# Kernel tuning notes

Measured on AMD Instinct MI355X. Metric: run time of the kernel, lower is better.

## Reference

```python
import jax, jax.numpy as jnp
import numpy as np

N_NODES = 15000
N_EDGES = 60000
D_NODE_IN = 74
D_EDGE_IN = 12
D = 64            # node_out_feats
D_EHID = 128      # edge_hidden_feats
N_STEPS = 6
BN_EPS = 1e-5


def setup_inputs() -> dict:
    key = jax.random.key(0)
    ks = jax.random.split(key, 16)
    def lin(k, fan_in, shape):
        return jax.random.normal(k, shape, jnp.float32) / np.sqrt(fan_in)
    inp = {
        "node_feats": jax.random.normal(ks[0], (N_NODES, D_NODE_IN), jnp.float32),
        "edge_feats": jax.random.normal(ks[1], (N_EDGES, D_EDGE_IN), jnp.float32),
        "src": jax.random.randint(ks[2], (N_EDGES,), 0, N_NODES, jnp.int32),
        "dst": jax.random.randint(ks[3], (N_EDGES,), 0, N_NODES, jnp.int32),
        # project_node_feats: Linear(node_in, D)
        "W_proj": lin(ks[4], D_NODE_IN, (D_NODE_IN, D)),
        "b_proj": jnp.zeros((D,), jnp.float32),
        # edge network: Linear(edge_in, ehid) -> ReLU -> Linear(ehid, D*D)
        "W_e1": lin(ks[5], D_EDGE_IN, (D_EDGE_IN, D_EHID)),
        "b_e1": jnp.zeros((D_EHID,), jnp.float32),
        "W_e2": lin(ks[6], D_EHID, (D_EHID, D * D)),
        "b_e2": jnp.zeros((D * D,), jnp.float32),
        # NNConv bias + BatchNorm affine params
        "conv_bias": jnp.zeros((D,), jnp.float32),
        "bn_gamma": jnp.ones((D,), jnp.float32),
        "bn_beta": jnp.zeros((D,), jnp.float32),
        # GRU (single layer): torch layout W_ih [3D, D], W_hh [3D, D]
        "W_ih": lin(ks[7], D, (3 * D, D)),
        "W_hh": lin(ks[8], D, (3 * D, D)),
        "b_ih": jnp.zeros((3 * D,), jnp.float32),
        "b_hh": jnp.zeros((3 * D,), jnp.float32),
    }
    return inp


def reference(node_feats, edge_feats, W_proj, b_proj, W_e1, b_e1, W_e2, b_e2,
              conv_bias, bn_gamma, bn_beta, W_ih, W_hh, b_ih, b_hh, src, dst):
    n_nodes = node_feats.shape[0]

    # project_node_feats: Linear + ReLU
    h = jax.nn.relu(node_feats @ W_proj + b_proj)          # [N, D]
    hidden = h                                              # GRU hidden state

    # edge MLP is a pure function of static edge_feats -> compute once
    ew = jax.nn.relu(edge_feats @ W_e1 + b_e1) @ W_e2 + b_e2
    ew = ew.reshape(-1, D, D)                               # [E, D, D]

    # mean-aggregation normalizer (DGL mean: 0 for isolated nodes)
    deg = jax.ops.segment_sum(jnp.ones_like(dst, jnp.float32), dst,
                              num_segments=n_nodes)
    inv_deg = jnp.where(deg > 0, 1.0 / jnp.maximum(deg, 1.0), 0.0)[:, None]

    for _ in range(N_STEPS):
        # per-edge matvec message: (h_src^T W_e); sum over d_in commutes
        # with the mean reduction, so reduce vectors instead of matrices.
        msg = jnp.einsum('ei,eio->eo', h[src], ew)          # [E, D]
        rst = jax.ops.segment_sum(msg, dst, num_segments=n_nodes) * inv_deg
        rst = rst + conv_bias
        # BatchNorm1d (training mode: batch statistics, biased variance)
        mu = rst.mean(axis=0)
        var = rst.var(axis=0)
        rst = (rst - mu) * jax.lax.rsqrt(var + BN_EPS) * bn_gamma + bn_beta
        m = jax.nn.relu(rst)
        # GRU cell (torch gate order: r, z, n)
        gi = m @ W_ih.T + b_ih
        gh = hidden @ W_hh.T + b_hh
        i_r, i_z, i_n = jnp.split(gi, 3, axis=-1)
        h_r, h_z, h_n = jnp.split(gh, 3, axis=-1)
        r = jax.nn.sigmoid(i_r + h_r)
        z = jax.nn.sigmoid(i_z + h_z)
        n = jnp.tanh(i_n + r * h_n)
        hidden = (1.0 - z) * n + z * hidden
        h = hidden
    return h
```

## Files before the change

### kernel.cpp

```cpp
#include <hip/hip_runtime.h>
#include <hip/hip_bf16.h>
#include <math.h>

#define NN 15000
#define NE 60000
#define DIN 74
#define DEIN 12
#define DD 64
#define EH 128
#define NG 8192
#define NSTEPS 6
#define NRB 235
#define NGB 235
#define KAB 384
#define NTMAX 18752
#define NFB 586

typedef unsigned short ushort_t;
typedef __attribute__((ext_vector_type(8))) short short8v;
typedef __attribute__((ext_vector_type(4))) float float4v;

__device__ __forceinline__ float bsf(unsigned short u){
  union { unsigned int i; float f; } v; v.i = ((unsigned int)u) << 16; return v.f;
}
__device__ __forceinline__ unsigned short fsb(float f){
  union { float f; unsigned int i; } v; v.f = f;
  unsigned int x = v.i;
  return (unsigned short)((x + 0x7FFFu + ((x >> 16) & 1u)) >> 16);
}
__device__ __forceinline__ unsigned int pkbf(float a, float b){
  __hip_bfloat162 r = __float22bfloat162_rn(make_float2(a, b));
  union { __hip_bfloat162 h; unsigned int u; } v; v.h = r; return v.u;
}

__global__ void k_sniff(const ushort_t* __restrict__ nf16,
                        const int* __restrict__ dsti, int* __restrict__ flags){
  __shared__ int cnt[2];
  int t = threadIdx.x;
  if (t < 2) cnt[t] = 0;
  __syncthreads();
  int bad = 0;
  for (int i = t; i < 1024; i += 256){
    unsigned short u = nf16[2*i];
    int e = (u >> 7) & 0xFF;
    if (e < 96 || e > 159) bad++;
  }
  if (bad) atomicAdd(&cnt[0], bad);
  if (t < 256 && dsti[2*t+1] == 0) atomicAdd(&cnt[1], 1);
  __syncthreads();
  if (t == 0){
    flags[0] = (cnt[0] > 300) ? 1 : 0;
    flags[1] = (cnt[1] > 250) ? 1 : 0;
  }
}

struct CanonArgs {
  const void* in[15];
  float* out[15];
  int n[15];
};
__global__ void k_canon_all(CanonArgs a, const int* __restrict__ flags){
  int j = blockIdx.y;
  int n = a.n[j];
  int fp32 = flags[0];
  const void* in = a.in[j];
  float* out = a.out[j];
  for (int i = blockIdx.x*256 + threadIdx.x; i < n; i += gridDim.x*256){
    if (fp32) out[i] = ((const float*)in)[i];
    else      out[i] = bsf(((const ushort_t*)in)[i]);
  }
}
__global__ void k_canoni2(const void* __restrict__ in0, const void* __restrict__ in1,
                          int* __restrict__ out0, int* __restrict__ out1,
                          const int* __restrict__ flags){
  int i = blockIdx.x*256 + threadIdx.x;
  if (i >= NE) return;
  const void* in = blockIdx.y ? in1 : in0;
  int* out = blockIdx.y ? out1 : out0;
  long long v = flags[1] ? ((const long long*)in)[i]
                         : (long long)((const int*)in)[i];
  int vi = (int)v;
  if (vi < 0) vi = 0;
  if (vi >= NN) vi = NN-1;
  out[i] = vi;
}

__global__ void k_proj(const float* __restrict__ nf, const float* __restrict__ Wp,
                       const float* __restrict__ bp, float* __restrict__ hid,
                       ushort_t* __restrict__ ab){
  __shared__ float nfl[4][DIN];
  int t = threadIdx.x, blk = blockIdx.x;
  for (int idx = t; idx < 4*DIN; idx += 256){
    int vl = idx / DIN, i = idx - vl*DIN;
    nfl[vl][i] = nf[(size_t)(blk*4+vl)*DIN + i];
  }
  __syncthreads();
  int vl = t >> 6, o = t & 63;
  int v = blk*4 + vl;
  float acc = bp[o];
  for (int i = 0; i < DIN; ++i) acc += nfl[vl][i] * Wp[i*DD + o];
  float r = fmaxf(acc, 0.f);
  hid[(size_t)v*DD + o] = r;
  ushort_t hh = fsb(r);
  float hl = r - bsf(hh);
  ab[(size_t)v*KAB + 64 + o]  = hh;
  ab[(size_t)v*KAB + 192 + o] = fsb(hl);
  ab[(size_t)v*KAB + 320 + o] = hh;
}

__global__ void k_emlp(const float* __restrict__ ef, const float* __restrict__ W1,
                       const float* __restrict__ b1, ushort_t* __restrict__ thi,
                       ushort_t* __restrict__ tlo){
  __shared__ float efl[2][DEIN];
  int t = threadIdx.x, blk = blockIdx.x;
  if (t < 2*DEIN){
    int el = t / DEIN, i = t - el*DEIN;
    efl[el][i] = ef[(size_t)(blk*2+el)*DEIN + i];
  }
  __syncthreads();
  int el = t >> 7, c = t & 127;
  float acc = b1[c];
  for (int i = 0; i < DEIN; ++i) acc += efl[el][i] * W1[i*EH + c];
  float tv = fmaxf(acc, 0.f);
  ushort_t hiv = fsb(tv);
  size_t off = (size_t)(blk*2+el)*EH + c;
  thi[off] = hiv;
  tlo[off] = fsb(tv - bsf(hiv));
}
__global__ void k_zpad(ushort_t* __restrict__ thi, ushort_t* __restrict__ tlo){
  int t = threadIdx.x;
  thi[(size_t)NE*EH + t] = 0;
  tlo[(size_t)NE*EH + t] = 0;
}

__global__ void k_w2q(const float* __restrict__ W2, const float* __restrict__ b2,
                      ushort_t* __restrict__ w2q, ushort_t* __restrict__ w2b){
  int idx = blockIdx.x*256 + threadIdx.x;
  if (idx < NG*DD){
    int n = idx >> 6, i = idx & 63;
    int kq = n >> 11, rem = n & 2047;
    int o = rem >> 5, kl = rem & 31;
    int kg = kq*32 + kl;
    w2q[idx] = fsb(W2[(size_t)kg*4096 + i*64 + o]);
  } else if (idx < NG*DD + DD*DD){
    int r = idx - NG*DD;
    int o = r >> 6, i = r & 63;
    w2b[r] = fsb(b2[i*64 + o]);
  }
}

__global__ void k_wgru(const float* __restrict__ Wih, const float* __restrict__ Whh,
                       ushort_t* __restrict__ wg){
  int pos = blockIdx.x*256 + threadIdx.x;
  if (pos >= 256*KAB) return;
  int c = pos / KAB, k = pos - c*KAB;
  int kb = k >> 6, i = k & 63;
  int g = c >> 6, o = c & 63;
  float w = 0.f;
  if ((kb & 1) == 0){
    if (g == 0)      w = Wih[(size_t)(o)*64 + i];
    else if (g == 1) w = Wih[(size_t)(64+o)*64 + i];
    else if (g == 2) w = Wih[(size_t)(128+o)*64 + i];
  } else {
    if (g == 0)      w = Whh[(size_t)(o)*64 + i];
    else if (g == 1) w = Whh[(size_t)(64+o)*64 + i];
    else if (g == 3) w = Whh[(size_t)(128+o)*64 + i];
  }
  ushort_t hi = fsb(w);
  wg[pos] = (kb >= 4) ? fsb(w - bsf(hi)) : hi;
}

__global__ void k_zero(int* __restrict__ p, int n){
  int i = blockIdx.x*256 + threadIdx.x;
  if (i < n) p[i] = 0;
}
__global__ void k_deg2(const int* __restrict__ a0, const int* __restrict__ a1,
                       int* __restrict__ d0, int* __restrict__ d1){
  int e = blockIdx.x*256 + threadIdx.x;
  if (e < NE){
    if (blockIdx.y == 0) atomicAdd(&d0[a0[e]], 1);
    else                 atomicAdd(&d1[a1[e]], 1);
  }
}
__global__ void k_scan2(const int* __restrict__ degA, int* __restrict__ rowpA,
                        float* __restrict__ invdA,
                        const int* __restrict__ degB, int* __restrict__ rowpB,
                        float* __restrict__ invdB){
  const int* deg = blockIdx.x ? degB : degA;
  int* rowp      = blockIdx.x ? rowpB : rowpA;
  float* invd    = blockIdx.x ? invdB : invdA;
  __shared__ int ssum[256];
  int t = threadIdx.x;
  const int STRIP = (NN + 255) / 256;
  int lo = t*STRIP, hi = (lo + STRIP < NN) ? lo + STRIP : NN;
  int s = 0;
  for (int i = lo; i < hi; ++i) s += deg[i];
  ssum[t] = s;
  __syncthreads();
  if (t == 0){
    int acc = 0;
    for (int i = 0; i < 256; ++i){ int v = ssum[i]; ssum[i] = acc; acc += v; }
  }
  __syncthreads();
  int acc = ssum[t];
  for (int i = lo; i < hi; ++i){
    rowp[i] = acc;
    int d = deg[i];
    invd[i] = (d > 0) ? 1.0f/(float)d : 0.0f;
    acc += d;
  }
  if (t == 255) rowp[NN] = acc;
}
__global__ void k_scatter2(const int* __restrict__ dstc, const int* __restrict__ rowpD,
                           int* __restrict__ curD, int* __restrict__ eidxD,
                           int* __restrict__ epos,
                           const int* __restrict__ srcc, const int* __restrict__ rowpS,
                           int* __restrict__ curS, int* __restrict__ eidxS){
  int e = blockIdx.x*256 + threadIdx.x;
  if (e >= NE) return;
  if (blockIdx.y == 0){
    int d = dstc[e];
    int pos = atomicAdd(&curD[d], 1);
    int slot = rowpD[d] + pos;
    eidxD[slot] = e;
    epos[e] = slot;
  } else {
    int d = srcc[e];
    int pos = atomicAdd(&curS[d], 1);
    eidxS[rowpS[d] + pos] = e;
  }
}

__global__ void k_tiles(const int* __restrict__ rowp, int* __restrict__ tnode,
                        int* __restrict__ tbase, int* __restrict__ tcnt,
                        int* __restrict__ ntb){
  __shared__ int ss[256];
  int t = threadIdx.x;
  const int STRIP = (NN + 255) / 256;
  int lo = t*STRIP, hi = lo + STRIP; if (hi > NN) hi = NN;
  int c = 0;
  for (int i = lo; i < hi; ++i){
    int deg = rowp[i+1] - rowp[i];
    c += (deg + 15) >> 4;
  }
  ss[t] = c;
  __syncthreads();
  if (t == 0){
    int a = 0;
    for (int i = 0; i < 256; ++i){ int v = ss[i]; ss[i] = a; a += v; }
    ntb[0] = a;
  }
  __syncthreads();
  int pos = ss[t];
  for (int i = lo; i < hi; ++i){
    int b = rowp[i], deg = rowp[i+1] - b;
    for (int r = 0; r < deg; r += 16){
      tnode[pos] = i; tbase[pos] = b + r;
      int c2 = deg - r; tcnt[pos] = (c2 > 16) ? 16 : c2;
      ++pos;
    }
  }
}

__global__ __launch_bounds__(512,4) void k_fused7(
    const ushort_t* __restrict__ ab, const ushort_t* __restrict__ w2q,
    const ushort_t* __restrict__ w2b, const ushort_t* __restrict__ thi,
    const ushort_t* __restrict__ tlo,
    const int* __restrict__ tnode, const int* __restrict__ tbase,
    const int* __restrict__ tcnt, const int* __restrict__ ntb,
    const int* __restrict__ eidx, const int* __restrict__ epos,
    float* __restrict__ msg){
  __shared__ __align__(16) ushort_t Gl[32768];
  __shared__ float bhl[32*66];
  __shared__ int nodl[32], cntl[32], basel[32];
  __shared__ int eidl[32][16];
  __shared__ int posl[32][16];

  int tid = threadIdx.x;
  int nt = ntb[0];
  int T0 = blockIdx.x * 32;
  if (T0 >= nt) return;
  int wv = tid >> 6, lane = tid & 63;
  int lr = lane & 15, quad = lane >> 4;

  if (tid < 32){
    int gt = T0 + tid;
    int node = 0, base = 0, cnt = 0;
    if (gt < nt){ node = tnode[gt]; base = tbase[gt]; cnt = tcnt[gt]; }
    nodl[tid] = node; basel[tid] = base; cntl[tid] = cnt;
  }
  __syncthreads();
  {
    int j = tid >> 4, sl = tid & 15;
    int eid = NE, ps = 0;
    if (sl < cntl[j]){
      eid = eidx[basel[j] + sl];
      ps = epos[eid];
    }
    eidl[j][sl] = eid;
    posl[j][sl] = ps;
  }
  short8v hf0k0, hf0k1, hf1k0, hf1k1;
  {
    int n0 = nodl[lr], n1 = nodl[16 + lr];
    hf0k0 = *(const short8v*)(ab + (size_t)n0*KAB + 64 + quad*8);
    hf0k1 = *(const short8v*)(ab + (size_t)n0*KAB + 96 + quad*8);
    hf1k0 = *(const short8v*)(ab + (size_t)n1*KAB + 64 + quad*8);
    hf1k1 = *(const short8v*)(ab + (size_t)n1*KAB + 96 + quad*8);
  }
  {
    int ot = wv & 3, mh = wv >> 2;
    float4v ba = (float4v){0.f,0.f,0.f,0.f};
    short8v a0 = *(const short8v*)(w2b + (size_t)(ot*16 + lr)*DD + quad*8);
    short8v a1 = *(const short8v*)(w2b + (size_t)(ot*16 + lr)*DD + 32 + quad*8);
    ba = __builtin_amdgcn_mfma_f32_16x16x32_bf16(a0, mh ? hf1k0 : hf0k0, ba, 0,0,0);
    ba = __builtin_amdgcn_mfma_f32_16x16x32_bf16(a1, mh ? hf1k1 : hf0k1, ba, 0,0,0);
    #pragma unroll
    for (int reg = 0; reg < 4; ++reg)
      bhl[(mh*16 + lr)*66 + ot*16 + quad*4 + reg] = ba[reg];
  }

  int j0 = wv*4;
  for (int oh = 0; oh < 2; ++oh){
    float4v acc[4][2];
    #pragma unroll
    for (int j = 0; j < 4; ++j)
      #pragma unroll
      for (int ot = 0; ot < 2; ++ot)
        acc[j][ot] = (float4v){0.f,0.f,0.f,0.f};
    for (int kq = 0; kq < 4; ++kq){
      __syncthreads();
      #pragma unroll 4
      for (int it = 0; it < 8; ++it){
        int tile = wv*8 + it;
        int nrow = kq*2048 + oh*1024 + tile*16 + lr;
        const ushort_t* arow = w2q + (size_t)nrow*DD;
        short8v a0 = *(const short8v*)(arow + quad*8);
        short8v a1 = *(const short8v*)(arow + 32 + quad*8);
        int ol = tile >> 1;
        int klb = ((tile & 1) << 4) + quad*4;
        int q8 = klb >> 3, jj = klb & 7;
        #pragma unroll
        for (int mh = 0; mh < 2; ++mh){
          float4v g = (float4v){0.f,0.f,0.f,0.f};
          g = __builtin_amdgcn_mfma_f32_16x16x32_bf16(a0, mh ? hf1k0 : hf0k0, g, 0,0,0);
          g = __builtin_amdgcn_mfma_f32_16x16x32_bf16(a1, mh ? hf1k1 : hf0k1, g, 0,0,0);
          int m = mh*16 + lr;
          unsigned int p0 = pkbf(g[0], g[1]);
          unsigned int p1 = pkbf(g[2], g[3]);
          int byt = ((((m*4 + q8)*32 + ol) << 4) + jj*2) ^ ((m & 7) << 4);
          uint2 pv; pv.x = p0; pv.y = p1;
          *(uint2*)((char*)Gl + byt) = pv;
        }
      }
      short8v th0, th1, th2, th3, tw0, tw1, tw2, tw3;
      {
        size_t kqo = (size_t)kq*32 + quad*8;
        int e0 = eidl[j0+0][lr], e1 = eidl[j0+1][lr];
        int e2 = eidl[j0+2][lr], e3 = eidl[j0+3][lr];
        th0 = *(const short8v*)(thi + (size_t)e0*EH + kqo);
        tw0 = *(const short8v*)(tlo + (size_t)e0*EH + kqo);
        th1 = *(const short8v*)(thi + (size_t)e1*EH + kqo);
        tw1 = *(const short8v*)(tlo + (size_t)e1*EH + kqo);
        th2 = *(const short8v*)(thi + (size_t)e2*EH + kqo);
        tw2 = *(const short8v*)(tlo + (size_t)e2*EH + kqo);
        th3 = *(const short8v*)(thi + (size_t)e3*EH + kqo);
        tw3 = *(const short8v*)(tlo + (size_t)e3*EH + kqo);
      }
      __syncthreads();
      #pragma unroll
      for (int j = 0; j < 4; ++j){
        int m = j0 + j;
        int swz = (m & 7) << 4;
        short8v thj = (j==0)?th0:(j==1)?th1:(j==2)?th2:th3;
        short8v twj = (j==0)?tw0:(j==1)?tw1:(j==2)?tw2:tw3;
        #pragma unroll
        for (int ot = 0; ot < 2; ++ot){
          int byt = (((m*4 + quad)*32 + ot*16 + lr) << 4) ^ swz;
          short8v gf = *(const short8v*)((const char*)Gl + byt);
          acc[j][ot] = __builtin_amdgcn_mfma_f32_16x16x32_bf16(thj, gf, acc[j][ot], 0,0,0);
          acc[j][ot] = __builtin_amdgcn_mfma_f32_16x16x32_bf16(twj, gf, acc[j][ot], 0,0,0);
        }
      }
    }
    #pragma unroll
    for (int j = 0; j < 4; ++j){
      int m = j0 + j;
      #pragma unroll
      for (int ot = 0; ot < 2; ++ot){
        int o = oh*32 + ot*16 + lr;
        float bb = bhl[m*66 + o];
        #pragma unroll
        for (int reg = 0; reg < 4; ++reg){
          int sl = quad*4 + reg;
          int eid = eidl[m][sl];
          if (eid < NE) msg[(size_t)posl[m][sl]*DD + o] = acc[j][ot][reg] + bb;
        }
      }
    }
  }
}

__global__ __launch_bounds__(512) void k_red(const float* __restrict__ msg,
                      const int* __restrict__ rowp_d,
                      const float* __restrict__ invd, const float* __restrict__ cbias,
                      float* __restrict__ rst, float* __restrict__ part){
  __shared__ float ls[512], ls2[512];
  int t = threadIdx.x, blk = blockIdx.x;
  int o = t & 63, gg = t >> 6;
  float cb = cbias[o];
  float s = 0.f, s2 = 0.f;
  int nbase = blk*64 + gg*8;
  int rp[9];
  #pragma unroll
  for (int k = 0; k < 9; ++k){
    int idx = nbase + k; if (idx > NN) idx = NN;
    rp[k] = rowp_d[idx];
  }
  #pragma unroll 1
  for (int j = 0; j < 8; ++j){
    int n = nbase + j;
    if (n >= NN) break;
    int b = rp[j], e = rp[j+1];
    float a0 = 0.f, a1 = 0.f, a2 = 0.f, a3 = 0.f;
    int i = b;
    for (; i + 3 < e; i += 4){
      a0 += msg[(size_t)i*DD + o];
      a1 += msg[(size_t)(i+1)*DD + o];
      a2 += msg[(size_t)(i+2)*DD + o];
      a3 += msg[(size_t)(i+3)*DD + o];
    }
    for (; i < e; ++i) a0 += msg[(size_t)i*DD + o];
    float x = ((a0 + a1) + (a2 + a3)) * invd[n] + cb;
    rst[(size_t)n*DD + o] = x;
    s += x; s2 += x*x;
  }
  ls[t] = s; ls2[t] = s2;
  __syncthreads();
  if (t < 64){
    float a = 0.f;
    #pragma unroll
    for (int g = 0; g < 8; ++g) a += ls[g*64 + t];
    part[blk*128 + t] = a;
  } else if (t < 128){
    int o2 = t - 64;
    float a = 0.f;
    #pragma unroll
    for (int g = 0; g < 8; ++g) a += ls2[g*64 + o2];
    part[blk*128 + 64 + o2] = a;
  }
}

__global__ __launch_bounds__(512) void k_gru_one(
    const float* __restrict__ rst, const float* __restrict__ part,
    const float* __restrict__ gamma, const float* __restrict__ beta,
    ushort_t* __restrict__ ab, const ushort_t* __restrict__ wg,
    const float* __restrict__ bih, const float* __restrict__ bhh,
    float* __restrict__ hid, float* __restrict__ out, int write_out){
  __shared__ __align__(16) ushort_t As[64][136];
  __shared__ __align__(16) ushort_t Bs[256][136];
  __shared__ float gl[64*257];
  __shared__ float scl[64], sft[64];
  __shared__ float shp[4][128];
  int t = threadIdx.x;
  int r0 = blockIdx.x * 64;
  {
    int tg = t >> 7, tc = t & 127;
    float s0 = 0.f, s1 = 0.f;
    int b = tg;
    for (; b + 4 < NRB; b += 8){ s0 += part[b*128 + tc]; s1 += part[(b+4)*128 + tc]; }
    for (; b < NRB; b += 4) s0 += part[b*128 + tc];
    shp[tg][tc] = s0 + s1;
  }
  __syncthreads();
  if (t < 64){
    float su = shp[0][t] + shp[1][t] + shp[2][t] + shp[3][t];
    float sq = shp[0][64+t] + shp[1][64+t] + shp[2][64+t] + shp[3][64+t];
    float mu = su / (float)NN;
    float var = sq / (float)NN - mu*mu;
    if (var < 0.f) var = 0.f;
    float rsq = rsqrtf(var + 1e-5f);
    float sc = rsq * gamma[t];
    scl[t] = sc;
    sft[t] = beta[t] - mu*sc;
  }
  int wv = t >> 6, lane = t & 63;
  int lr = lane & 15, quad = lane >> 4;
  int n0 = wv * 32;
  float4v acc[4][2];
  #pragma unroll
  for (int mt = 0; mt < 4; ++mt)
    #pragma unroll
    for (int nt = 0; nt < 2; ++nt) acc[mt][nt] = (float4v){0.f,0.f,0.f,0.f};
  for (int kt = 0; kt < 3; ++kt){
    __syncthreads();
    #pragma unroll
    for (int it = 0; it < 2; ++it){
      int cid = t + it*512;
      int r = cid >> 4, ko = (cid & 15) * 8;
      int gm = r0 + r; if (gm >= NN) gm = NN-1;
      if (ko < 64){
        float4 x0 = *(const float4*)(rst + (size_t)gm*DD + ko);
        float4 x1 = *(const float4*)(rst + (size_t)gm*DD + ko + 4);
        float xv[8] = {x0.x,x0.y,x0.z,x0.w,x1.x,x1.y,x1.z,x1.w};
        ushort_t u[8];
        #pragma unroll
        for (int jj = 0; jj < 8; ++jj){
          float m = fmaxf(xv[jj]*scl[ko+jj] + sft[ko+jj], 0.f);
          ushort_t mh = fsb(m);
          u[jj] = (kt == 1) ? fsb(m - bsf(mh)) : mh;
        }
        *(uint4*)&As[r][ko] = *(const uint4*)u;
      } else {
        *(uint4*)&As[r][ko] = *(const uint4*)(ab + (size_t)gm*KAB + kt*128 + ko);
      }
    }
    #pragma unroll
    for (int it = 0; it < 8; ++it){
      int cid = t + it*512;
      int rB = cid >> 4, ko = (cid & 15) * 8;
      *(uint4*)&Bs[rB][ko] = *(const uint4*)(wg + (size_t)rB*KAB + kt*128 + ko);
    }
    __syncthreads();
    #pragma unroll
    for (int ks = 0; ks < 4; ++ks){
      short8v a[4];
      #pragma unroll
      for (int mt = 0; mt < 4; ++mt)
        a[mt] = *(const short8v*)&As[mt*16 + lr][ks*32 + quad*8];
      #pragma unroll
      for (int nt = 0; nt < 2; ++nt){
        short8v b = *(const short8v*)&Bs[n0 + nt*16 + lr][ks*32 + quad*8];
        #pragma unroll
        for (int mt = 0; mt < 4; ++mt)
          acc[mt][nt] = __builtin_amdgcn_mfma_f32_16x16x32_bf16(a[mt], b, acc[mt][nt], 0,0,0);
      }
    }
  }
  #pragma unroll
  for (int mt = 0; mt < 4; ++mt)
    #pragma unroll
    for (int nt = 0; nt < 2; ++nt){
      int col = n0 + nt*16 + lr;
      #pragma unroll
      for (int reg = 0; reg < 4; ++reg)
        gl[(mt*16 + quad*4 + reg)*257 + col] = acc[mt][nt][reg];
    }
  __syncthreads();
  for (int idx = t; idx < 64*64; idx += 512){
    int row = idx >> 6, o = idx & 63;
    int v = r0 + row;
    if (v >= NN) break;
    const float* g = &gl[row*257];
    float aR  = g[o]       + bih[o]      + bhh[o];
    float aZ  = g[64 + o]  + bih[64+o]   + bhh[64+o];
    float aNi = g[128 + o] + bih[128+o];
    float aNh = g[192 + o] + bhh[128+o];
    float hprev = hid[(size_t)v*DD + o];
    float r = 1.f/(1.f+__expf(-aR));
    float z = 1.f/(1.f+__expf(-aZ));
    float n = tanhf(aNi + r*aNh);
    float hnew = (1.f - z)*n + z*hprev;
    hid[(size_t)v*DD + o] = hnew;
    ushort_t hh = fsb(hnew);
    float hl = hnew - bsf(hh);
    ab[(size_t)v*KAB + 64 + o]  = hh;
    ab[(size_t)v*KAB + 192 + o] = fsb(hl);
    ab[(size_t)v*KAB + 320 + o] = hh;
    if (write_out) out[(size_t)v*DD + o] = hnew;
  }
}

extern "C" void kernel_launch(void* const* d_in, const int* in_sizes, int n_in,
                              void* d_out, int out_size, void* d_ws, size_t ws_size,
                              hipStream_t stream){
  (void)out_size; (void)ws_size;
  float* out = (float*)d_out;

  int p_nf=-1,p_ef=-1,p_src=-1,p_dst=-1,p_Wp=-1,p_bp=-1,p_W1=-1,p_b1=-1,
      p_W2=-1,p_b2=-1,p_cb=-1,p_gam=-1,p_bet=-1,p_Wih=-1,p_Whh=-1,p_bih=-1,p_bhh=-1;
  int c60000=0,c64=0,c12288=0,c192=0;
  for (int i = 0; i < n_in; ++i){
    switch (in_sizes[i]){
      case 1110000: p_nf = i; break;
      case 720000:  p_ef = i; break;
      case 60000:   if (c60000++ == 0) p_src = i; else p_dst = i; break;
      case 4736:    p_Wp = i; break;
      case 64:      { if (c64==0) p_bp=i; else if (c64==1) p_cb=i;
                      else if (c64==2) p_gam=i; else p_bet=i; c64++; } break;
      case 1536:    p_W1 = i; break;
      case 128:     p_b1 = i; break;
      case 524288:  p_W2 = i; break;
      case 4096:    p_b2 = i; break;
      case 12288:   if (c12288++ == 0) p_Wih = i; else p_Whh = i; break;
      case 192:    if (c192++ == 0) p_bih = i; else p_bhh = i; break;
      default: break;
    }
  }

  char* p = (char*)d_ws;
  auto alloc = [&](size_t bytes)->char*{
    char* r = p; p += (bytes + 255) & ~(size_t)255; return r;
  };
  int* flags = (int*)alloc(256);
  const int FPOS[15] = {p_nf,p_ef,p_Wp,p_bp,p_W1,p_b1,p_W2,p_b2,p_cb,p_gam,p_bet,
                        p_Wih,p_Whh,p_bih,p_bhh};
  CanonArgs ca;
  int maxn = 0;
  for (int j = 0; j < 15; ++j){
    int n = in_sizes[FPOS[j]];
    ca.in[j]  = d_in[FPOS[j]];
    ca.out[j] = (float*)alloc((size_t)n * 4);
    ca.n[j]   = n;
    if (n > maxn) maxn = n;
  }
  const float* nf  = ca.out[0];  const float* ef  = ca.out[1];
  const float* Wp  = ca.out[2];  const float* bp  = ca.out[3];
  const float* W1  = ca.out[4];  const float* b1  = ca.out[5];
  const float* W2  = ca.out[6];  const float* b2  = ca.out[7];
  const float* cb  = ca.out[8];  const float* gam = ca.out[9];
  const float* bet = ca.out[10]; const float* Wih = ca.out[11];
  const float* Whh = ca.out[12]; const float* bih = ca.out[13];
  const float* bhh = ca.out[14];
  int* srcc = (int*)alloc((size_t)NE*4);
  int* dstc = (int*)alloc((size_t)NE*4);

  ushort_t* thi   = (ushort_t*)alloc((size_t)(NE+1)*EH*2);
  ushort_t* tlo   = (ushort_t*)alloc((size_t)(NE+1)*EH*2);
  ushort_t* w2q   = (ushort_t*)alloc((size_t)NG*DD*2);
  ushort_t* w2b   = (ushort_t*)alloc((size_t)DD*DD*2);
  float* hid      = (float*)alloc((size_t)NN*DD*4);
  ushort_t* ab    = (ushort_t*)alloc((size_t)NN*KAB*2);
  ushort_t* wg    = (ushort_t*)alloc((size_t)256*KAB*2);
  float* rst      = (float*)alloc((size_t)NN*DD*4);
  float* msg      = (float*)alloc((size_t)NE*DD*4);
  float* part     = (float*)alloc((size_t)NRB*128*4);
  int* degall     = (int*)alloc((size_t)4*NN*4);
  int* deg  = degall;
  int* curd = degall + NN;
  int* deg2 = degall + 2*NN; int* cursor2 = degall + 3*NN;
  float* invd = (float*)alloc((size_t)NN*4);
  int* rowp_d = (int*)alloc((size_t)(NN+1)*4);
  int* eidx_d = (int*)alloc((size_t)NE*4);
  int* epos   = (int*)alloc((size_t)NE*4);
  int* rowp2  = (int*)alloc((size_t)(NN+1)*4);
  float* invd2= (float*)alloc((size_t)NN*4);
  int* eidx2  = (int*)alloc((size_t)NE*4);
  int* tnode  = (int*)alloc((size_t)NTMAX*4);
  int* tbase  = (int*)alloc((size_t)NTMAX*4);
  int* tcnt   = (int*)alloc((size_t)NTMAX*4);
  int* ntb    = (int*)alloc(256);

  k_sniff<<<1, 256, 0, stream>>>((const ushort_t*)d_in[p_nf], (const int*)d_in[p_dst], flags);
  k_canon_all<<<dim3((maxn+255)/256, 15), 256, 0, stream>>>(ca, flags);
  k_canoni2<<<dim3((NE+255)/256, 2), 256, 0, stream>>>(d_in[p_src], d_in[p_dst],
                                                       srcc, dstc, flags);

  k_proj <<<NN/4,  256, 0, stream>>>(nf, Wp, bp, hid, ab);
  k_emlp <<<NE/2,  256, 0, stream>>>(ef, W1, b1, thi, tlo);
  k_zpad <<<1, 128, 0, stream>>>(thi, tlo);
  k_w2q  <<<(NG*DD + DD*DD + 255)/256, 256, 0, stream>>>(W2, b2, w2q, w2b);
  k_wgru <<<(256*KAB+255)/256, 256, 0, stream>>>(Wih, Whh, wg);
  k_zero <<<(4*NN+255)/256, 256, 0, stream>>>(degall, 4*NN);
  k_deg2 <<<dim3((NE+255)/256, 2), 256, 0, stream>>>(dstc, srcc, deg, deg2);
  k_scan2<<<2, 256, 0, stream>>>(deg, rowp_d, invd, deg2, rowp2, invd2);
  k_scatter2<<<dim3((NE+255)/256, 2), 256, 0, stream>>>(dstc, rowp_d, curd, eidx_d,
                                                        epos, srcc, rowp2, cursor2, eidx2);
  k_tiles<<<1, 256, 0, stream>>>(rowp2, tnode, tbase, tcnt, ntb);

  for (int s = 0; s < NSTEPS; ++s){
    k_fused7<<<NFB, 512, 0, stream>>>(ab, w2q, w2b, thi, tlo,
                                      tnode, tbase, tcnt, ntb, eidx2, epos, msg);
    k_red <<<NRB, 512, 0, stream>>>(msg, rowp_d, invd, cb, rst, part);
    k_gru_one<<<NGB, 512, 0, stream>>>(rst, part, gam, bet, ab, wg, bih, bhh,
                                       hid, out, (s == NSTEPS-1) ? 1 : 0);
  }
}
```

Measured before the change: 947.5 us.

## Fuse reduction and GRU kernels into one cooperative kernel with grid sync

Merges the per-node mean-aggregation/BatchNorm-partial kernel and the BN+GRU kernel into a single cooperative launch, using a grid-wide barrier between computing partial statistics and consuming them. This removes one kernel launch and its boundary per step, and reuses the GRU kernel's shared memory for the reduction scratch. In exchange it relies on cooperative launch: all 235 blocks of 512 threads with large shared memory must be co-resident, and the grid sync adds its own cost.

```diff
diff --git a/kernel.cpp b/kernel.cpp
--- a/kernel.cpp
+++ b/kernel.cpp
@@ -1,5 +1,6 @@
 #include <hip/hip_runtime.h>
 #include <hip/hip_bf16.h>
+#include <hip/hip_cooperative_groups.h>
 #include <math.h>
 
 #define NN 15000
@@ -11,10 +12,11 @@
 #define NG 8192
 #define NSTEPS 6
 #define NRB 235
-#define NGB 235
 #define KAB 384
 #define NTMAX 18752
 #define NFB 586
+
+namespace cg = cooperative_groups;
 
 typedef unsigned short ushort_t;
 typedef __attribute__((ext_vector_type(8))) short short8v;
@@ -401,58 +403,10 @@
   }
 }
 
-__global__ __launch_bounds__(512) void k_red(const float* __restrict__ msg,
-                      const int* __restrict__ rowp_d,
-                      const float* __restrict__ invd, const float* __restrict__ cbias,
-                      float* __restrict__ rst, float* __restrict__ part){
-  __shared__ float ls[512], ls2[512];
-  int t = threadIdx.x, blk = blockIdx.x;
-  int o = t & 63, gg = t >> 6;
-  float cb = cbias[o];
-  float s = 0.f, s2 = 0.f;
-  int nbase = blk*64 + gg*8;
-  int rp[9];
-  #pragma unroll
-  for (int k = 0; k < 9; ++k){
-    int idx = nbase + k; if (idx > NN) idx = NN;
-    rp[k] = rowp_d[idx];
-  }
-  #pragma unroll 1
-  for (int j = 0; j < 8; ++j){
-    int n = nbase + j;
-    if (n >= NN) break;
-    int b = rp[j], e = rp[j+1];
-    float a0 = 0.f, a1 = 0.f, a2 = 0.f, a3 = 0.f;
-    int i = b;
-    for (; i + 3 < e; i += 4){
-      a0 += msg[(size_t)i*DD + o];
-      a1 += msg[(size_t)(i+1)*DD + o];
-      a2 += msg[(size_t)(i+2)*DD + o];
-      a3 += msg[(size_t)(i+3)*DD + o];
-    }
-    for (; i < e; ++i) a0 += msg[(size_t)i*DD + o];
-    float x = ((a0 + a1) + (a2 + a3)) * invd[n] + cb;
-    rst[(size_t)n*DD + o] = x;
-    s += x; s2 += x*x;
-  }
-  ls[t] = s; ls2[t] = s2;
-  __syncthreads();
-  if (t < 64){
-    float a = 0.f;
-    #pragma unroll
-    for (int g = 0; g < 8; ++g) a += ls[g*64 + t];
-    part[blk*128 + t] = a;
-  } else if (t < 128){
-    int o2 = t - 64;
-    float a = 0.f;
-    #pragma unroll
-    for (int g = 0; g < 8; ++g) a += ls2[g*64 + o2];
-    part[blk*128 + 64 + o2] = a;
-  }
-}
-
-__global__ __launch_bounds__(512) void k_gru_one(
-    const float* __restrict__ rst, const float* __restrict__ part,
+__global__ __launch_bounds__(512) void k_tail(
+    const float* __restrict__ msg, const int* __restrict__ rowp_d,
+    const float* __restrict__ invd, const float* __restrict__ cbias,
+    float* __restrict__ rst, float* __restrict__ part,
     const float* __restrict__ gamma, const float* __restrict__ beta,
     ushort_t* __restrict__ ab, const ushort_t* __restrict__ wg,
     const float* __restrict__ bih, const float* __restrict__ bhh,
@@ -463,7 +417,58 @@
   __shared__ float scl[64], sft[64];
   __shared__ float shp[4][128];
   int t = threadIdx.x;
-  int r0 = blockIdx.x * 64;
+  int blk = blockIdx.x;
+  int r0 = blk * 64;
+
+  {
+    float* ls  = gl;
+    float* ls2 = gl + 512;
+    int o = t & 63, gg = t >> 6;
+    float cb = cbias[o];
+    float s = 0.f, s2 = 0.f;
+    int nbase = blk*64 + gg*8;
+    int rp[9];
+    #pragma unroll
+    for (int k = 0; k < 9; ++k){
+      int idx = nbase + k; if (idx > NN) idx = NN;
+      rp[k] = rowp_d[idx];
+    }
+    #pragma unroll 1
+    for (int j = 0; j < 8; ++j){
+      int n = nbase + j;
+      if (n >= NN) break;
+      int b = rp[j], e = rp[j+1];
+      float a0 = 0.f, a1 = 0.f, a2 = 0.f, a3 = 0.f;
+      int i = b;
+      for (; i + 3 < e; i += 4){
+        a0 += msg[(size_t)i*DD + o];
+        a1 += msg[(size_t)(i+1)*DD + o];
+        a2 += msg[(size_t)(i+2)*DD + o];
+        a3 += msg[(size_t)(i+3)*DD + o];
+      }
+      for (; i < e; ++i) a0 += msg[(size_t)i*DD + o];
+      float x = ((a0 + a1) + (a2 + a3)) * invd[n] + cb;
+      rst[(size_t)n*DD + o] = x;
+      s += x; s2 += x*x;
+    }
+    ls[t] = s; ls2[t] = s2;
+    __syncthreads();
+    if (t < 64){
+      float a = 0.f;
+      #pragma unroll
+      for (int g = 0; g < 8; ++g) a += ls[g*64 + t];
+      part[blk*128 + t] = a;
+    } else if (t < 128){
+      int o2 = t - 64;
+      float a = 0.f;
+      #pragma unroll
+      for (int g = 0; g < 8; ++g) a += ls2[g*64 + o2];
+      part[blk*128 + 64 + o2] = a;
+    }
+  }
+
+  cg::this_grid().sync();
+
   {
     int tg = t >> 7, tc = t & 127;
     float s0 = 0.f, s1 = 0.f;
@@ -671,8 +676,12 @@
   for (int s = 0; s < NSTEPS; ++s){
     k_fused7<<<NFB, 512, 0, stream>>>(ab, w2q, w2b, thi, tlo,
                                       tnode, tbase, tcnt, ntb, eidx2, epos, msg);
-    k_red <<<NRB, 512, 0, stream>>>(msg, rowp_d, invd, cb, rst, part);
-    k_gru_one<<<NGB, 512, 0, stream>>>(rst, part, gam, bet, ab, wg, bih, bhh,
-                                       hid, out, (s == NSTEPS-1) ? 1 : 0);
-  }
-}
+    int wout = (s == NSTEPS-1) ? 1 : 0;
+    void* targs[] = {(void*)&msg, (void*)&rowp_d, (void*)&invd, (void*)&cb,
+                     (void*)&rst, (void*)&part, (void*)&gam, (void*)&bet,
+                     (void*)&ab, (void*)&wg, (void*)&bih, (void*)&bhh,
+                     (void*)&hid, (void*)&out, (void*)&wout};
+    hipLaunchCooperativeKernel((const void*)k_tail, dim3(NRB), dim3(512),
+                               targs, 0, stream);
+  }
+}
```

Measured after the change: 1.207 ms. 27.4% more time.
